# Performance work log

Hardware: AMD Instinct MI355X
Metric: run time of the kernel (lower is better)

## Reference

```python
import jax, jax.numpy as jnp
import numpy as np

N_QUBITS = 10
EMBED_DIM = 512
FFN_DIM = 2048
DIM = 2 ** N_QUBITS


def _apply_rx(state, theta, wire):
    # state: (N, 2^n) complex64; theta: scalar or (N,)
    N = state.shape[0]
    hi = 2 ** wire                      # dims before the wire axis (wire 0 = MSB)
    lo = 2 ** (N_QUBITS - 1 - wire)
    s = state.reshape(N, hi, 2, lo)
    th = jnp.asarray(theta, jnp.float32).reshape(-1, 1, 1)  # (N,1,1) or (1,1,1)
    c = jnp.cos(th / 2).astype(jnp.complex64)
    ms = (-1j * jnp.sin(th / 2)).astype(jnp.complex64)
    s0, s1 = s[:, :, 0, :], s[:, :, 1, :]
    out = jnp.stack([c * s0 + ms * s1, ms * s0 + c * s1], axis=2)
    return out.reshape(N, DIM)


def _apply_cnot(state, ctrl, tgt):
    N = state.shape[0]
    s = state.reshape((N,) + (2,) * N_QUBITS)
    s0 = jax.lax.index_in_dim(s, 0, axis=ctrl + 1, keepdims=True)
    s1 = jax.lax.index_in_dim(s, 1, axis=ctrl + 1, keepdims=True)
    s1 = jnp.flip(s1, axis=tgt + 1)  # X on target where control == 1
    return jnp.concatenate([s0, s1], axis=ctrl + 1).reshape(N, DIM)


def _pauliz_signs():
    idx = np.arange(DIM)
    bits = (idx[:, None] >> (N_QUBITS - 1 - np.arange(N_QUBITS))[None, :]) & 1
    return jnp.asarray(1.0 - 2.0 * bits, jnp.float32)  # (2^n, n)


def _quantum_layer(tokens, rx_params):
    # tokens: (N, embed_dim); uses first n_qubits features as encoder angles
    N = tokens.shape[0]
    state = jnp.zeros((N, DIM), jnp.complex64).at[:, 0].set(1.0)
    for w in range(N_QUBITS):                    # encoder: RX(x_w) on wire w
        state = _apply_rx(state, tokens[:, w], w)
    for w in range(N_QUBITS):                    # trainable RX per wire
        state = _apply_rx(state, rx_params[w], w)
    for w in range(N_QUBITS - 1):                # CNOT chain
        state = _apply_cnot(state, w, w + 1)
    state = _apply_cnot(state, N_QUBITS - 1, 0)  # wrap-around CNOT
    probs = state.real ** 2 + state.imag ** 2    # (N, 2^n)
    return probs @ _pauliz_signs()               # (N, n_qubits) <Z_w>


def setup_inputs() -> dict:
    key = jax.random.key(0)
    ks = jax.random.split(key, 6)
    x = jax.random.normal(ks[0], (16, 1024, EMBED_DIM), jnp.float32)
    rx_params = jax.random.normal(ks[1], (N_QUBITS,), jnp.float32)
    lim1 = 1.0 / np.sqrt(N_QUBITS)
    w1 = jax.random.uniform(ks[2], (FFN_DIM, N_QUBITS), jnp.float32, -lim1, lim1)
    b1 = jax.random.uniform(ks[3], (FFN_DIM,), jnp.float32, -lim1, lim1)
    lim2 = 1.0 / np.sqrt(FFN_DIM)
    w2 = jax.random.uniform(ks[4], (EMBED_DIM, FFN_DIM), jnp.float32, -lim2, lim2)
    b2 = jax.random.uniform(ks[5], (EMBED_DIM,), jnp.float32, -lim2, lim2)
    return {"x": x, "rx_params": rx_params, "w1": w1, "b1": b1, "w2": w2, "b2": b2}


def reference(x, rx_params, w1, b1, w2, b2):
    B, S, _ = x.shape
    q_out = _quantum_layer(x.reshape(B * S, EMBED_DIM), rx_params)
    q_out = q_out.reshape(B, S, N_QUBITS)
    h = jax.nn.relu(q_out @ w1.T + b1)           # dropout is identity in eval
    return h @ w2.T + b2
```

## Files before the change

### kernel.cpp

```cpp
#include <hip/hip_runtime.h>
#include <hip/hip_bf16.h>
#include <math.h>


typedef __attribute__((ext_vector_type(8))) short short8;
typedef __attribute__((ext_vector_type(8))) unsigned short ushort8;
typedef __attribute__((ext_vector_type(4))) float fx4;

constexpr int EDIM = 512;
constexpr int FDIM = 2048;
constexpr int NQ   = 10;
constexpr int BK   = 64;
constexpr int BM   = 128;
constexpr int BN   = 128;

__device__ __forceinline__ ushort f2bf(float f) {
    union { float f; unsigned u; } v; v.f = f;
    unsigned u = v.u + 0x7FFFu + ((v.u >> 16) & 1u);
    return (ushort)(u >> 16);
}
__device__ __forceinline__ float bf2f(ushort u) {
    union { unsigned u; float f; } v; v.u = (unsigned)u << 16; return v.f;
}
__device__ __forceinline__ unsigned bits2(__hip_bfloat162 h) {
    union { __hip_bfloat162 h; unsigned u; } v; v.h = h; return v.u;
}
__device__ __forceinline__ unsigned cvtpk(float lo, float hi) {
    unsigned r;
    asm("v_cvt_pk_bf16_f32 %0, %1, %2" : "=v"(r) : "v"(lo), "v"(hi));
    return r;
}
__device__ __forceinline__ void gload_lds16(const void* g, void* l) {
    __builtin_amdgcn_global_load_lds(
        (const __attribute__((address_space(1))) void*)g,
        (__attribute__((address_space(3))) void*)l, 16, 0, 0);
}

__global__ void prep(const float* __restrict__ w2, const float* __restrict__ w1,
                     const float* __restrict__ b1,
                     ushort* __restrict__ w2b, ushort* __restrict__ w1t) {
    int gid = blockIdx.x * blockDim.x + threadIdx.x;
    int np  = gridDim.x * blockDim.x;
    for (int i = gid; i < EDIM * FDIM / 4; i += np) {
        float4 v = ((const float4*)w2)[i];
        ushort4 o; o.x = f2bf(v.x); o.y = f2bf(v.y); o.z = f2bf(v.z); o.w = f2bf(v.w);
        ((ushort4*)w2b)[i] = o;
    }
    for (int f = gid; f < FDIM; f += np) {
        ushort zr[32];
        #pragma unroll
        for (int w = 0; w < NQ; ++w) {
            float v  = w1[f * NQ + w];
            ushort hb = f2bf(v);
            ushort lb = f2bf(v - bf2f(hb));
            zr[w] = hb; zr[10 + w] = hb; zr[20 + w] = lb;
        }
        float bv  = b1[f];
        ushort bh = f2bf(bv);
        zr[30] = bh; zr[31] = f2bf(bv - bf2f(bh));
        #pragma unroll
        for (int u = 0; u < 4; ++u)
            *(ushort8*)&w1t[f * 32 + u * 8] = *(ushort8*)&zr[u * 8];
    }
}

__global__ __launch_bounds__(256, 2) void fused(
    const float* __restrict__ x, const float* __restrict__ rx,
    const ushort* __restrict__ w1t,
    const ushort* __restrict__ w2b,
    const float* __restrict__ b2,
    float* __restrict__ out)
{
    __shared__ __align__(16) ushort Zs[BM * 32];
    __shared__ __align__(16) ushort As[2][BM * BK];
    __shared__ __align__(16) ushort Bs[2][BN * BK];

    const int tid = threadIdx.x;
    const int m0  = blockIdx.x * BM;
    const int n0  = blockIdx.y * BN;

    if (tid < BM) {
        const float* xr = x + (size_t)(m0 + tid) * EDIM;
        float4 xa = *(const float4*)xr;
        float4 xb = *(const float4*)(xr + 4);
        float2 xc = *(const float2*)(xr + 8);
        float xv[NQ] = {xa.x, xa.y, xa.z, xa.w, xb.x, xb.y, xb.z, xb.w, xc.x, xc.y};
        float c[NQ], q[NQ];
        #pragma unroll
        for (int w = 0; w < NQ; ++w) c[w] = cosf(xv[w] + rx[w]);
        float p0 = c[1];
        #pragma unroll
        for (int w = 2; w < NQ; ++w) p0 *= c[w];
        q[0] = p0;
        float p = c[0];
        #pragma unroll
        for (int w = 1; w < NQ; ++w) { p *= c[w]; q[w] = p; }
        ushort zr[32];
        #pragma unroll
        for (int w = 0; w < NQ; ++w) {
            ushort hb = f2bf(q[w]);
            ushort lb = f2bf(q[w] - bf2f(hb));
            zr[w] = hb; zr[10 + w] = lb; zr[20 + w] = hb;
        }
        zr[30] = 0x3F80u; zr[31] = 0x3F80u;
        #pragma unroll
        for (int u = 0; u < 4; ++u)
            *(ushort8*)&Zs[tid * 32 + u * 8] = *(ushort8*)&zr[u * 8];
    }
    __syncthreads();

    const int wave = tid >> 6, lane = tid & 63;
    const int quad = lane >> 4, l16 = lane & 15;
    const int wm   = wave >> 1, wn = wave & 1;
    const int swz  = l16 & 7;

    const int hm0 = (wave & 1) * 64;
    const int hf0 = (wave >> 1) * 32;
    short8 zf[4];
    #pragma unroll
    for (int mi = 0; mi < 4; ++mi)
        zf[mi] = *(const short8*)&Zs[(hm0 + mi * 16 + l16) * 32 + quad * 8];

    const int srow0 = tid >> 3;
    const int sbs   = tid & 7;
    const ushort* gB[4];
    #pragma unroll
    for (int u = 0; u < 4; ++u) {
        int row = u * 32 + srow0;
        int bl  = sbs ^ (row & 7);
        gB[u] = w2b + (size_t)(n0 + row) * FDIM + bl * 8;
    }
    const int ldst = wave * 512;

    int aro[4], bro[4];
    #pragma unroll
    for (int t = 0; t < 4; ++t) {
        aro[t] = (wm * 64 + t * 16 + l16) * BK;
        bro[t] = (wn * 64 + t * 16 + l16) * BK;
    }

    fx4 acc[4][4];
    #pragma unroll
    for (int a = 0; a < 4; ++a)
        #pragma unroll
        for (int b = 0; b < 4; ++b) acc[a][b] = fx4{0.f, 0.f, 0.f, 0.f};

    const fx4 zacc = fx4{0.f, 0.f, 0.f, 0.f};

    short8 wfE[2], wfO[2];
    uint2  pE[4][2], pO[4][2];

#define WLOAD(WF, CH) do { _Pragma("unroll") \
    for (int fi = 0; fi < 2; ++fi) \
        WF[fi] = *(const short8*)(w1t + ((CH) * 64 + hf0 + fi * 16 + l16) * 32 + quad * 8); \
} while (0)

#define STAGEB(BUF) do { _Pragma("unroll") \
    for (int u = 0; u < 4; ++u) { gload_lds16(gB[u], &Bs[BUF][u * 2048 + ldst]); gB[u] += BK; } \
} while (0)

#define HCALC(P, WF) do { _Pragma("unroll") \
    for (int mi = 0; mi < 4; ++mi) \
        _Pragma("unroll") \
        for (int fi = 0; fi < 2; ++fi) { \
            fx4 hv = __builtin_amdgcn_mfma_f32_16x16x32_bf16( \
                WF[fi], zf[mi], zacc, 0, 0, 0); \
            unsigned ua = cvtpk(fmaxf(hv[0], 0.f), fmaxf(hv[1], 0.f)); \
            unsigned ub = cvtpk(fmaxf(hv[2], 0.f), fmaxf(hv[3], 0.f)); \
            P[mi][fi] = make_uint2(ua, ub); \
        } \
} while (0)

#define HWRITE(BUF, P) do { _Pragma("unroll") \
    for (int mi = 0; mi < 4; ++mi) { \
        const int hrow = hm0 + mi * 16 + l16; \
        ushort* arow = &As[BUF][hrow * BK]; \
        _Pragma("unroll") \
        for (int fi = 0; fi < 2; ++fi) { \
            const int blk = (hf0 >> 3) + fi * 2 + (quad >> 1); \
            *(uint2*)&arow[((blk ^ swz) << 3) + ((quad & 1) << 2)] = P[mi][fi]; \
        } \
    } \
} while (0)

#define COMPUTE(BUF) do { \
    short8 af[4][2], bf[4][2]; \
    _Pragma("unroll") \
    for (int t = 0; t < 4; ++t) \
        _Pragma("unroll") \
        for (int hf = 0; hf < 2; ++hf) { \
            const int blkb = (((hf * 4 + quad) ^ swz) << 3); \
            af[t][hf] = *(const short8*)&As[BUF][aro[t] + blkb]; \
            bf[t][hf] = *(const short8*)&Bs[BUF][bro[t] + blkb]; \
        } \
    __builtin_amdgcn_s_setprio(1); \
    _Pragma("unroll") \
    for (int hf = 0; hf < 2; ++hf) \
        _Pragma("unroll") \
        for (int mt = 0; mt < 4; ++mt) \
            _Pragma("unroll") \
            for (int nt = 0; nt < 4; ++nt) \
                acc[mt][nt] = __builtin_amdgcn_mfma_f32_16x16x32_bf16( \
                    af[mt][hf], bf[nt][hf], acc[mt][nt], 0, 0, 0); \
    __builtin_amdgcn_s_setprio(0); \
} while (0)

    WLOAD(wfE, 0); WLOAD(wfO, 1);
    STAGEB(0);
    HCALC(pE, wfE); HWRITE(0, pE);
    HCALC(pO, wfO);
    WLOAD(wfE, 2); WLOAD(wfO, 3);
    __syncthreads();

    for (int p = 0; p < 14; ++p) {
        STAGEB(1); HWRITE(1, pO); HCALC(pE, wfE); WLOAD(wfE, 2 * p + 4);
        COMPUTE(0); __syncthreads();
        STAGEB(0); HWRITE(0, pE); HCALC(pO, wfO); WLOAD(wfO, 2 * p + 5);
        COMPUTE(1); __syncthreads();
    }
    STAGEB(1); HWRITE(1, pO); HCALC(pE, wfE);
    COMPUTE(0); __syncthreads();
    STAGEB(0); HWRITE(0, pE); HCALC(pO, wfO);
    COMPUTE(1); __syncthreads();
    STAGEB(1); HWRITE(1, pO);
    COMPUTE(0); __syncthreads();
    COMPUTE(1);

#undef COMPUTE
#undef HWRITE
#undef HCALC
#undef STAGEB
#undef WLOAD

    float bb[4];
    #pragma unroll
    for (int nt = 0; nt < 4; ++nt) bb[nt] = b2[n0 + wn * 64 + nt * 16 + l16];
    #pragma unroll
    for (int mt = 0; mt < 4; ++mt) {
        const int mbase = m0 + wm * 64 + mt * 16 + quad * 4;
        #pragma unroll
        for (int nt = 0; nt < 4; ++nt) {
            const int n = n0 + wn * 64 + nt * 16 + l16;
            #pragma unroll
            for (int r = 0; r < 4; ++r)
                out[(size_t)(mbase + r) * EDIM + n] = acc[mt][nt][r] + bb[nt];
        }
    }
}

extern "C" void kernel_launch(void* const* d_in, const int* in_sizes, int n_in,
                              void* d_out, int out_size, void* d_ws, size_t ws_size,
                              hipStream_t stream) {
    const float* x  = (const float*)d_in[0];
    const float* rx = (const float*)d_in[1];
    const float* w1 = (const float*)d_in[2];
    const float* b1 = (const float*)d_in[3];
    const float* w2 = (const float*)d_in[4];
    const float* b2 = (const float*)d_in[5];
    float* out = (float*)d_out;

    const int M = in_sizes[0] / EDIM;

    ushort* w2b = (ushort*)d_ws;
    ushort* w1t = (ushort*)((char*)d_ws + (size_t)EDIM * FDIM * 2);
    (void)ws_size; (void)n_in; (void)out_size;

    hipLaunchKernelGGL(prep, dim3(256), dim3(256), 0, stream, w2, w1, b1, w2b, w1t);
    hipLaunchKernelGGL(fused, dim3(M / BM, EDIM / BN), dim3(256), 0, stream,
                       x, rx, w1t, w2b, b2, out);
}
```

Baseline: 132.8 us.

## Load W2 fragments directly from global into registers instead of staging through LDS

Replaces the global-to-LDS async staging of the W2 tile with direct per-wave global loads of MFMA B fragments into double-buffered registers. This removes the Bs shared-memory buffers and the matching LDS reads, which cuts LDS traffic and footprint. In exchange each wave now reads its own B fragments from global/L2 without sharing through LDS, so global traffic goes up, and the extra register-held fragments raise register pressure under launch_bounds(256,2).

```diff
diff --git a/kernel.cpp b/kernel.cpp
--- a/kernel.cpp
+++ b/kernel.cpp
@@ -22,18 +22,10 @@
 __device__ __forceinline__ float bf2f(ushort u) {
     union { unsigned u; float f; } v; v.u = (unsigned)u << 16; return v.f;
 }
-__device__ __forceinline__ unsigned bits2(__hip_bfloat162 h) {
-    union { __hip_bfloat162 h; unsigned u; } v; v.h = h; return v.u;
-}
 __device__ __forceinline__ unsigned cvtpk(float lo, float hi) {
     unsigned r;
     asm("v_cvt_pk_bf16_f32 %0, %1, %2" : "=v"(r) : "v"(lo), "v"(hi));
     return r;
-}
-__device__ __forceinline__ void gload_lds16(const void* g, void* l) {
-    __builtin_amdgcn_global_load_lds(
-        (const __attribute__((address_space(1))) void*)g,
-        (__attribute__((address_space(3))) void*)l, 16, 0, 0);
 }
 
 __global__ void prep(const float* __restrict__ w2, const float* __restrict__ w1,
@@ -73,7 +65,6 @@
 {
     __shared__ __align__(16) ushort Zs[BM * 32];
     __shared__ __align__(16) ushort As[2][BM * BK];
-    __shared__ __align__(16) ushort Bs[2][BN * BK];
 
     const int tid = threadIdx.x;
     const int m0  = blockIdx.x * BM;
@@ -121,23 +112,15 @@
     for (int mi = 0; mi < 4; ++mi)
         zf[mi] = *(const short8*)&Zs[(hm0 + mi * 16 + l16) * 32 + quad * 8];
 
-    const int srow0 = tid >> 3;
-    const int sbs   = tid & 7;
-    const ushort* gB[4];
-    #pragma unroll
-    for (int u = 0; u < 4; ++u) {
-        int row = u * 32 + srow0;
-        int bl  = sbs ^ (row & 7);
-        gB[u] = w2b + (size_t)(n0 + row) * FDIM + bl * 8;
-    }
-    const int ldst = wave * 512;
-
-    int aro[4], bro[4];
-    #pragma unroll
-    for (int t = 0; t < 4; ++t) {
+    const ushort* gBF[4];
+    #pragma unroll
+    for (int nt = 0; nt < 4; ++nt)
+        gBF[nt] = w2b + (size_t)(n0 + wn * 64 + nt * 16 + l16) * FDIM + quad * 8;
+
+    int aro[4];
+    #pragma unroll
+    for (int t = 0; t < 4; ++t)
         aro[t] = (wm * 64 + t * 16 + l16) * BK;
-        bro[t] = (wn * 64 + t * 16 + l16) * BK;
-    }
 
     fx4 acc[4][4];
     #pragma unroll
@@ -149,14 +132,19 @@
 
     short8 wfE[2], wfO[2];
     uint2  pE[4][2], pO[4][2];
+    short8 bfE[4][2], bfO[4][2];
 
 #define WLOAD(WF, CH) do { _Pragma("unroll") \
     for (int fi = 0; fi < 2; ++fi) \
         WF[fi] = *(const short8*)(w1t + ((CH) * 64 + hf0 + fi * 16 + l16) * 32 + quad * 8); \
 } while (0)
 
-#define STAGEB(BUF) do { _Pragma("unroll") \
-    for (int u = 0; u < 4; ++u) { gload_lds16(gB[u], &Bs[BUF][u * 2048 + ldst]); gB[u] += BK; } \
+#define BLOAD(BFR) do { _Pragma("unroll") \
+    for (int nt = 0; nt < 4; ++nt) { \
+        BFR[nt][0] = *(const short8*)(gBF[nt]); \
+        BFR[nt][1] = *(const short8*)(gBF[nt] + 32); \
+        gBF[nt] += BK; \
+    } \
 } while (0)
 
 #define HCALC(P, WF) do { _Pragma("unroll") \
@@ -183,16 +171,13 @@
     } \
 } while (0)
 
-#define COMPUTE(BUF) do { \
-    short8 af[4][2], bf[4][2]; \
+#define COMPUTE(BUF, BFR) do { \
+    short8 af[4][2]; \
     _Pragma("unroll") \
     for (int t = 0; t < 4; ++t) \
         _Pragma("unroll") \
-        for (int hf = 0; hf < 2; ++hf) { \
-            const int blkb = (((hf * 4 + quad) ^ swz) << 3); \
-            af[t][hf] = *(const short8*)&As[BUF][aro[t] + blkb]; \
-            bf[t][hf] = *(const short8*)&Bs[BUF][bro[t] + blkb]; \
-        } \
+        for (int hf = 0; hf < 2; ++hf) \
+            af[t][hf] = *(const short8*)&As[BUF][aro[t] + (((hf * 4 + quad) ^ swz) << 3)]; \
     __builtin_amdgcn_s_setprio(1); \
     _Pragma("unroll") \
     for (int hf = 0; hf < 2; ++hf) \
@@ -201,35 +186,42 @@
             _Pragma("unroll") \
             for (int nt = 0; nt < 4; ++nt) \
                 acc[mt][nt] = __builtin_amdgcn_mfma_f32_16x16x32_bf16( \
-                    af[mt][hf], bf[nt][hf], acc[mt][nt], 0, 0, 0); \
+                    af[mt][hf], BFR[nt][hf], acc[mt][nt], 0, 0, 0); \
     __builtin_amdgcn_s_setprio(0); \
 } while (0)
 
     WLOAD(wfE, 0); WLOAD(wfO, 1);
-    STAGEB(0);
+    BLOAD(bfE);
     HCALC(pE, wfE); HWRITE(0, pE);
     HCALC(pO, wfO);
     WLOAD(wfE, 2); WLOAD(wfO, 3);
     __syncthreads();
 
     for (int p = 0; p < 14; ++p) {
-        STAGEB(1); HWRITE(1, pO); HCALC(pE, wfE); WLOAD(wfE, 2 * p + 4);
-        COMPUTE(0); __syncthreads();
-        STAGEB(0); HWRITE(0, pE); HCALC(pO, wfO); WLOAD(wfO, 2 * p + 5);
-        COMPUTE(1); __syncthreads();
-    }
-    STAGEB(1); HWRITE(1, pO); HCALC(pE, wfE);
-    COMPUTE(0); __syncthreads();
-    STAGEB(0); HWRITE(0, pE); HCALC(pO, wfO);
-    COMPUTE(1); __syncthreads();
-    STAGEB(1); HWRITE(1, pO);
-    COMPUTE(0); __syncthreads();
-    COMPUTE(1);
+        BLOAD(bfO);
+        HWRITE(1, pO); HCALC(pE, wfE); WLOAD(wfE, 2 * p + 4);
+        COMPUTE(0, bfE);
+        __syncthreads();
+        BLOAD(bfE);
+        HWRITE(0, pE); HCALC(pO, wfO); WLOAD(wfO, 2 * p + 5);
+        COMPUTE(1, bfO);
+        __syncthreads();
+    }
+    BLOAD(bfO);
+    HWRITE(1, pO); HCALC(pE, wfE);
+    COMPUTE(0, bfE); __syncthreads();
+    BLOAD(bfE);
+    HWRITE(0, pE); HCALC(pO, wfO);
+    COMPUTE(1, bfO); __syncthreads();
+    BLOAD(bfO);
+    HWRITE(1, pO);
+    COMPUTE(0, bfE); __syncthreads();
+    COMPUTE(1, bfO);
 
 #undef COMPUTE
 #undef HWRITE
 #undef HCALC
-#undef STAGEB
+#undef BLOAD
 #undef WLOAD
 
     float bb[4];
```

After: 158.9 us. 19.7% more time.
